# Kernel optimization log

Measured on AMD Instinct MI355X. Metric: run time of the kernel, lower is better.

Reference implementation:

```python
import jax, jax.numpy as jnp
import numpy as np
import math

B, T, C, TF, N, DK = 4, 2048, 768, 128, 8, 96  # DK = max(C//8,16)

def _tau_init(Tw):
    alpha = 0.1 ** (1.0 / max(Tw - 1, 1))
    tau = -math.log(max(alpha, 1e-10))
    return math.log(math.exp(tau) - 1 + 1e-10)

def setup_inputs() -> dict:
    key = jax.random.key(0)
    ks = jax.random.split(key, 13)
    w = lambda k, shp: jax.random.normal(k, shp, jnp.float32) * 0.02
    return {
        'x': jax.random.normal(ks[0], (B, T, C), jnp.float32),
        'tau_gate': jnp.float32(_tau_init(max(T // 2, 4))),
        'tau_fast': jnp.float32(_tau_init(TF)),
        'tau_slow': jnp.float32(_tau_init(T)),
        'Wp': w(ks[1], (C, C)), 'bp': jnp.zeros((C,), jnp.float32),
        'Wxf': w(ks[2], (C, C)), 'bxf': jnp.full((C,), -0.5, jnp.float32),
        'Wxs': w(ks[3], (C, C)), 'bxs': jnp.full((C,), 0.5, jnp.float32),
        'Wcf': w(ks[4], (C, C)), 'Wcs': w(ks[5], (C, C)),
        'Wq': w(ks[6], (DK, C)), 'Wk': w(ks[7], (DK, C)),
        'Wfast': w(ks[8], (C, C)), 'bfast': jnp.zeros((C,), jnp.float32),
        'Wslow': w(ks[9], (C, C)), 'bslow': jnp.zeros((C,), jnp.float32),
        'Wsoma': w(ks[10], (C, C)), 'bsoma': jnp.zeros((C,), jnp.float32),
        'Wanc': w(ks[11], (C, C)), 'banc': jnp.zeros((C,), jnp.float32),
        'anchor_scales': jnp.linspace(1.5, -1.5, N).astype(jnp.float32),
        'blend_raw': jnp.zeros((1,), jnp.float32),
        'ln_g': jnp.ones((C,), jnp.float32), 'ln_b': jnp.zeros((C,), jnp.float32),
    }

def _lin(x, W, b=None):
    # torch Linear: y = x @ W.T + b, W is (out, in)
    y = jnp.einsum('btc,oc->bto', x, W)
    return y if b is None else y + b

def _ema(b, tau_raw):
    # exact h_t = alpha*h_{t-1} + b_t, h_{-1}=0 (same math as full causal conv with kernel alpha^j)
    alpha = jnp.exp(-jax.nn.softplus(tau_raw))
    def step(h, bt):
        h = alpha * h + bt
        return h, h
    _, hs = jax.lax.scan(step, jnp.zeros_like(b[:, 0, :]), jnp.swapaxes(b, 0, 1))
    return jnp.swapaxes(hs, 0, 1)  # (B,T,C)

def _forward(x, tau_gate, tau_fast, tau_slow, Wp, bp, Wxf, bxf, Wxs, bxs, Wcf, Wcs,
             Wq, Wk, Wfast, bfast, Wslow, bslow, Wsoma, bsoma, Wanc, banc,
             anchor_scales, blend_raw, ln_g, ln_b):
    x_proj = jnp.tanh(_lin(x, Wp, bp))
    ctx_gate = _ema(x, tau_gate)
    wg_f = jax.nn.sigmoid(_lin(x, Wxf, bxf) + _lin(ctx_gate, Wcf))
    wg_s = jax.nn.sigmoid(_lin(x, Wxs, bxs) + _lin(ctx_gate, Wcs))
    ctx_fast = _ema(x_proj * wg_f, tau_fast)
    ctx_slow = _ema(x_proj * wg_s, tau_slow)
    # F1 content gate: causal max-score sigmoid
    q = _lin(x, Wq)
    k = _lin(x, Wk)
    sc = jnp.einsum('btd,bsd->bts', q, k) * (DK ** -0.5)
    tril = jnp.tril(jnp.ones((T, T), bool))
    sc = jnp.where(tril[None], sc, -jnp.inf)
    cg = jax.nn.sigmoid(jnp.max(sc, axis=-1, keepdims=True))  # (B,T,1)
    ctx_fast = ctx_fast * cg
    ctx_slow = ctx_slow * cg
    # F5 anchors (static positions)
    pos = np.array([min(i * (T // N), T - 1) for i in range(N)])
    a = jnp.tanh(jnp.einsum('bnc,oc->bno', x[:, pos, :], Wanc) + banc)  # (B,N,C)
    delta = jnp.einsum('n,bnc->bc', jax.nn.sigmoid(anchor_scales), a)
    ctx_fast = ctx_fast + delta[:, None, :]
    ctx_slow = ctx_slow + delta[:, None, :]
    # F6 blend of fast/slow gates (torch.lerp)
    bl = jax.nn.sigmoid(blend_raw)  # (1,)
    gf = jax.nn.sigmoid(_lin(ctx_fast, Wfast, bfast))
    gs = jax.nn.sigmoid(_lin(ctx_slow, Wslow, bslow))
    gate = gf + bl * (gs - gf)
    soma = jnp.tanh(_lin(x, Wsoma, bsoma))
    y = soma * gate
    mu = jnp.mean(y, -1, keepdims=True)
    var = jnp.var(y, -1, keepdims=True)
    return (y - mu) / jnp.sqrt(var + 1e-5) * ln_g + ln_b  # dropout p=0 -> identity

def reference(x, tau_gate, tau_fast, tau_slow, Wp, bp, Wxf, bxf, Wxs, bxs, Wcf, Wcs,
              Wq, Wk, Wfast, bfast, Wslow, bslow, Wsoma, bsoma, Wanc, banc,
              anchor_scales, blend_raw, ln_g, ln_b):
    return _forward(x, tau_gate, tau_fast, tau_slow, Wp, bp, Wxf, bxf, Wxs, bxs, Wcf, Wcs,
                    Wq, Wk, Wfast, bfast, Wslow, bslow, Wsoma, bsoma, Wanc, banc,
                    anchor_scales, blend_raw, ln_g, ln_b)
```

## Files before the change

### kernel.cpp

```cpp
#include <hip/hip_runtime.h>
#include <math.h>

#define B_ 4
#define T_ 2048
#define C_ 768
#define DK_ 96
#define NA_ 8
#define M_ (B_*T_)
#define K2_ (2*C_)
#define NCH_ 256
#define CK_ 8

typedef __attribute__((ext_vector_type(8))) _Float16 half8;
typedef __attribute__((ext_vector_type(4))) _Float16 half4;
typedef __attribute__((ext_vector_type(4))) float floatx4;

#define AS1 __attribute__((address_space(1)))
#define AS3 __attribute__((address_space(3)))

__device__ __forceinline__ float sigm(float x){ return 1.f/(1.f + expf(-x)); }
__device__ __forceinline__ unsigned enc_max(float f){
  unsigned i = __float_as_uint(f);
  return (i & 0x80000000u) ? ~i : (i | 0x80000000u);
}
__device__ __forceinline__ float dec_max(unsigned u){
  unsigned i = (u & 0x80000000u) ? (u & 0x7FFFFFFFu) : ~u;
  return __uint_as_float(i);
}
__device__ __forceinline__ void gld16(const _Float16* g, _Float16* l){
  __builtin_amdgcn_global_load_lds((const AS1 unsigned int*)g, (AS3 unsigned int*)l, 16, 0, 0);
}

__global__ __launch_bounds__(192) void k_castx(
    const float* __restrict__ x, const float* __restrict__ tau,
    _Float16* __restrict__ xh, float* __restrict__ Sg){
  float al = expf(-log1pf(expf(tau[0])));
  int blk = blockIdx.x, b = blk >> 8, ch = blk & (NCH_-1);
  int t0 = b*T_ + ch*CK_;
  int c4 = threadIdx.x;
  float s0=0.f,s1=0.f,s2=0.f,s3=0.f;
  #pragma unroll
  for (int t = 0; t < CK_; ++t){
    float4 v = *(const float4*)(x + (size_t)(t0+t)*C_ + c4*4);
    half4 h = { (_Float16)v.x,(_Float16)v.y,(_Float16)v.z,(_Float16)v.w };
    *(half4*)(xh + (size_t)(t0+t)*C_ + c4*4) = h;
    s0 = al*s0 + v.x; s1 = al*s1 + v.y; s2 = al*s2 + v.z; s3 = al*s3 + v.w;
  }
  float4 sv = { s0,s1,s2,s3 };
  *(float4*)(Sg + (size_t)blk*C_ + c4*4) = sv;
}

#define NB0 4608
#define NB1 4896
#define NB2 4920
#define NB3 4932
__global__ __launch_bounds__(256) void k_prep(
    const float* __restrict__ x,
    const float* __restrict__ Wp, const float* __restrict__ Wfast,
    const float* __restrict__ Wslow, const float* __restrict__ Wsoma,
    const float* __restrict__ Wxf, const float* __restrict__ Wxs,
    const float* __restrict__ Wcf, const float* __restrict__ Wcs,
    const float* __restrict__ Wq, const float* __restrict__ Wk,
    const float* __restrict__ Wanc, const float* __restrict__ banc,
    const float* __restrict__ ascl, const float* __restrict__ tau_gate,
    const float* __restrict__ Sg,
    _Float16* __restrict__ wall, _Float16* __restrict__ wqk,
    unsigned* __restrict__ cgE, float* __restrict__ Hg, float* __restrict__ dlt)
{
  __shared__ float xs[NA_*C_];
  __shared__ float part[NA_*128];
  int blk = blockIdx.x, tid = threadIdx.x;
  if (blk < NB0){
    int i = blk*256 + tid;
    const int per = (C_*C_)/4;
    int s = i / per, j = i - s*per;
    const float* src = s==0?Wp : s==1?Wfast : s==2?Wslow : s==3?Wsoma
                     : s==4?Wxf : s==5?Wxs : s==6?Wcf : Wcs;
    float4 v = ((const float4*)src)[j];
    half4 h = { (_Float16)v.x, (_Float16)v.y, (_Float16)v.z, (_Float16)v.w };
    ((half4*)wall)[(size_t)s*per + j] = h;
  } else if (blk < NB1){
    int sub = blk - NB0;
    if (sub >= 256){ cgE[(sub-256)*256 + tid] = 0u; return; }
    const float* src = (sub < 96) ? Wq + (size_t)sub*C_
                     : (sub < 192 ? Wk + (size_t)(sub-96)*C_ : nullptr);
    #pragma unroll
    for (int k = 0; k < 3; ++k){
      int c = tid + k*256;
      wqk[(size_t)sub*C_ + c] = src ? (_Float16)src[c] : (_Float16)0.f;
    }
  } else if (blk < NB2){
    int ab = blk - NB1;
    int ct = ab % 6, b = ab / 6;
    for (int i = tid; i < NA_*C_; i += 256){
      int n = i / C_, c = i - n*C_;
      xs[i] = x[(size_t)(b*T_ + n*(T_/NA_))*C_ + c];
    }
    __syncthreads();
    int col = ct*128 + (tid & 127), kh = tid >> 7;
    float acc[NA_] = {0,0,0,0,0,0,0,0};
    const float* wrow = Wanc + (size_t)col*C_ + kh*384;
    const float* xk = xs + kh*384;
    for (int k = 0; k < 384; ++k){
      float wv = wrow[k];
      #pragma unroll
      for (int n = 0; n < NA_; ++n) acc[n] += xk[n*C_ + k]*wv;
    }
    if (kh){
      #pragma unroll
      for (int n = 0; n < NA_; ++n) part[n*128 + (tid & 127)] = acc[n];
    }
    __syncthreads();
    if (!kh){
      float d = 0.f;
      float bv = banc[col];
      #pragma unroll
      for (int n = 0; n < NA_; ++n){
        float a = tanhf(acc[n] + part[n*128 + (tid & 127)] + bv);
        d += sigm(ascl[n]) * a;
      }
      dlt[(size_t)b*C_ + col] = d;
    }
  } else {
    int sub = blk - NB2;
    int b = sub / 3, c = (sub - b*3)*256 + tid;
    float aCK = expf(-(float)CK_ * log1pf(expf(tau_gate[0])));
    float h = 0.f;
    for (int ch = 0; ch < NCH_; ++ch){
      size_t idx = (size_t)(b*NCH_ + ch)*C_ + c;
      Hg[idx] = h;
      h = aCK*h + Sg[idx];
    }
  }
}

__global__ __launch_bounds__(256) void k_p2_fs(const float* __restrict__ Sf, const float* __restrict__ Ss,
                                               float* __restrict__ Hf, float* __restrict__ Hs,
                                               const float* __restrict__ tf, const float* __restrict__ ts){
  int blk = blockIdx.x;
  int which = blk / 12, sub = blk - which*12;
  int b = sub / 3, c = (sub - b*3)*256 + threadIdx.x;
  const float* S = which ? Ss : Sf;
  float* H = which ? Hs : Hf;
  float aCK = expf(-(float)CK_ * log1pf(expf(which ? ts[0] : tf[0])));
  float h = 0.f;
  for (int ch = 0; ch < NCH_; ++ch){
    size_t idx = (size_t)(b*NCH_ + ch)*C_ + c;
    H[idx] = h;
    h = aCK*h + S[idx];
  }
}

__global__ __launch_bounds__(192) void k_gate_p3(
    const _Float16* __restrict__ xh, const float* __restrict__ H,
    const float* __restrict__ tau, _Float16* __restrict__ gate){
  float al = expf(-log1pf(expf(tau[0])));
  int blk = blockIdx.x, b = blk >> 8, ch = blk & (NCH_-1);
  int c4 = threadIdx.x;
  float4 h0 = *(const float4*)(H + (size_t)blk*C_ + c4*4);
  float g0=h0.x, g1=h0.y, g2=h0.z, g3=h0.w;
  int t0 = b*T_ + ch*CK_;
  #pragma unroll
  for (int t = 0; t < CK_; ++t){
    half4 v = *(const half4*)(xh + (size_t)(t0+t)*C_ + c4*4);
    g0 = al*g0 + (float)v[0]; g1 = al*g1 + (float)v[1];
    g2 = al*g2 + (float)v[2]; g3 = al*g3 + (float)v[3];
    half4 o = { (_Float16)g0,(_Float16)g1,(_Float16)g2,(_Float16)g3 };
    *(half4*)(gate + (size_t)(t0+t)*C_ + c4*4) = o;
  }
}

__device__ __forceinline__ void stage_tile(const _Float16* __restrict__ src, int stride,
                                           int r0, int k0, _Float16* lds){
  int tid = threadIdx.x;
  int wave = tid >> 6, lane = tid & 63;
  #pragma unroll
  for (int it = 0; it < 4; ++it){
    int cb = it*256 + wave*64;
    int ck = cb + lane;
    int row = ck >> 3;
    int kp = (ck & 7) ^ (row & 7);
    gld16(src + (size_t)(r0+row)*stride + k0 + kp*8, lds + (size_t)cb*8);
  }
}

__device__ __forceinline__ void mfma_pass(const _Float16* As, const _Float16* Ws, floatx4 acc[4][4]){
  int tid = threadIdx.x;
  int wave = tid >> 6, lane = tid & 63;
  int wr = wave >> 1, wc = wave & 1;
  int lr = lane & 15, lq = lane >> 4;
  #pragma unroll
  for (int ks = 0; ks < 2; ++ks){
    half8 fa[4], fb[4];
    int off = (((ks*4 + lq) ^ (lr & 7)) << 3);
    #pragma unroll
    for (int i = 0; i < 4; ++i){
      fa[i] = *(const half8*)(As + (wr*64 + i*16 + lr)*64 + off);
      fb[i] = *(const half8*)(Ws + (wc*64 + i*16 + lr)*64 + off);
    }
    #pragma unroll
    for (int i = 0; i < 4; ++i)
      #pragma unroll
      for (int j = 0; j < 4; ++j)
        acc[i][j] = __builtin_amdgcn_mfma_f32_16x16x32_f16(fa[i], fb[j], acc[i][j], 0, 0, 0);
  }
}

__device__ __forceinline__ void store_tile_f16(floatx4 acc[4][4], _Float16* __restrict__ out, int ldo,
                                               const float* bias, const float* bias2,
                                               int m0, int n0, int act){
  int tid = threadIdx.x;
  int wave = tid >> 6, lane = tid & 63;
  int wr = wave >> 1, wc = wave & 1;
  int lr = lane & 15, lq = lane >> 4;
  #pragma unroll
  for (int i = 0; i < 4; ++i){
    #pragma unroll
    for (int j = 0; j < 4; ++j){
      int col = n0 + wc*64 + j*16 + lr;
      float bv = 0.f;
      if (bias) bv = (bias2 && col >= C_) ? bias2[col - C_] : bias[col];
      #pragma unroll
      for (int r = 0; r < 4; ++r){
        int rowm = m0 + wr*64 + i*16 + lq*4 + r;
        float z = acc[i][j][r] + bv;
        if (act == 1) z = tanhf(z);
        else if (act == 2) z = sigm(z);
        out[(size_t)rowm*ldo + col] = (_Float16)z;
      }
    }
  }
}

__global__ __launch_bounds__(256,4) void k_gemm_s3(
    const _Float16* __restrict__ xh, const _Float16* __restrict__ gate,
    const _Float16* __restrict__ wall, const _Float16* __restrict__ wqk,
    const float* __restrict__ bp, const float* __restrict__ bxf, const float* __restrict__ bxs,
    _Float16* __restrict__ xph, _Float16* __restrict__ wgfs, _Float16* __restrict__ qk)
{
  __shared__ _Float16 As[128*64];
  __shared__ _Float16 Ws[128*64];
  const size_t per = (size_t)C_*C_;
  floatx4 acc[4][4] = {};
  int m0 = blockIdx.x * 128;
  int ny = blockIdx.y;
  if (ny < 6){
    for (int k0 = 0; k0 < C_; k0 += 64){
      stage_tile(xh, C_, m0, k0, As);
      stage_tile(wall, C_, ny*128, k0, Ws);
      asm volatile("s_waitcnt vmcnt(0)" ::: "memory");
      __syncthreads();
      mfma_pass(As, Ws, acc);
      __syncthreads();
    }
    store_tile_f16(acc, xph, C_, bp, nullptr, m0, ny*128, 1);
  } else if (ny < 18){
    int n0 = (ny-6)*128;
    for (int k0 = 0; k0 < C_; k0 += 64){
      stage_tile(xh, C_, m0, k0, As);
      stage_tile(wall + 4*per, C_, n0, k0, Ws);
      asm volatile("s_waitcnt vmcnt(0)" ::: "memory");
      __syncthreads();
      mfma_pass(As, Ws, acc);
      __syncthreads();
    }
    for (int k0 = 0; k0 < C_; k0 += 64){
      stage_tile(gate, C_, m0, k0, As);
      stage_tile(wall + 6*per, C_, n0, k0, Ws);
      asm volatile("s_waitcnt vmcnt(0)" ::: "memory");
      __syncthreads();
      mfma_pass(As, Ws, acc);
      __syncthreads();
    }
    store_tile_f16(acc, wgfs, K2_, bxf, bxs, m0, n0, 2);
  } else {
    int n0 = (ny-18)*128;
    for (int k0 = 0; k0 < C_; k0 += 64){
      stage_tile(xh, C_, m0, k0, As);
      stage_tile(wqk, C_, n0, k0, Ws);
      asm volatile("s_waitcnt vmcnt(0)" ::: "memory");
      __syncthreads();
      mfma_pass(As, Ws, acc);
      __syncthreads();
    }
    store_tile_f16(acc, qk, 256, nullptr, nullptr, m0, n0, 0);
  }
}

__global__ __launch_bounds__(256,3) void k_gemm_s7(
    const _Float16* __restrict__ xph, const _Float16* __restrict__ wgfs,
    const _Float16* __restrict__ xh, const _Float16* __restrict__ wall,
    const float* __restrict__ Hf, const float* __restrict__ Hs,
    const float* __restrict__ tau_fast, const float* __restrict__ tau_slow,
    const unsigned* __restrict__ cgE, const float* __restrict__ dlt,
    const float* __restrict__ bf, const float* __restrict__ bs, const float* __restrict__ bso,
    _Float16* __restrict__ gfb, _Float16* __restrict__ gsb, _Float16* __restrict__ somab)
{
  __shared__ _Float16 As[128*64];
  __shared__ _Float16 Wg[128*64];
  __shared__ _Float16 Bs[128*64];
  __shared__ float cgv[128];
  const size_t per = (size_t)C_*C_;
  floatx4 acc[4][4] = {};
  int m0 = blockIdx.x * 128;
  int s = blockIdx.y / 6, nt = (blockIdx.y % 6) * 128;
  int tid = threadIdx.x;
  if (s == 2){
    for (int k0 = 0; k0 < C_; k0 += 64){
      stage_tile(xh, C_, m0, k0, As);
      stage_tile(wall + 3*per, C_, nt, k0, Bs);
      asm volatile("s_waitcnt vmcnt(0)" ::: "memory");
      __syncthreads();
      mfma_pass(As, Bs, acc);
      __syncthreads();
    }
    store_tile_f16(acc, somab, C_, bso, nullptr, m0, nt, 1);
  } else {
    float al = expf(-log1pf(expf(s ? tau_slow[0] : tau_fast[0])));
    const float* Hx = s ? Hs : Hf;
    const _Float16* wsrc = wgfs + (s ? C_ : 0);
    const _Float16* Wm = wall + (size_t)(s+1)*per;
    int b = m0 >> 11;
    int ch0 = (m0 & (T_-1)) >> 3;
    if (tid < 128) cgv[tid] = sigm(dec_max(cgE[m0 + tid]));
    __syncthreads();
    int rc = tid >> 4, cc = (tid >> 1) & 7, hh = tid & 1;
    for (int k0 = 0; k0 < C_; k0 += 64){
      stage_tile(xph, C_, m0, k0, As);
      stage_tile(wsrc, K2_, m0, k0, Wg);
      stage_tile(Wm, C_, nt, k0, Bs);
      asm volatile("s_waitcnt vmcnt(0)" ::: "memory");
      __syncthreads();
      {
        float4 hv = *(const float4*)(Hx + ((size_t)b*NCH_ + ch0 + rc)*C_ + k0 + cc*8 + hh*4);
        float4 d  = *(const float4*)(dlt + (size_t)b*C_ + k0 + cc*8 + hh*4);
        float e0=hv.x, e1=hv.y, e2=hv.z, e3=hv.w;
        #pragma unroll
        for (int r = 0; r < 8; ++r){
          int idx = (rc*8+r)*64 + ((cc^r)<<3) + hh*4;
          half4 p = *(const half4*)(As+idx);
          half4 wv = *(const half4*)(Wg+idx);
          e0 = al*e0 + (float)p[0]*(float)wv[0];
          e1 = al*e1 + (float)p[1]*(float)wv[1];
          e2 = al*e2 + (float)p[2]*(float)wv[2];
          e3 = al*e3 + (float)p[3]*(float)wv[3];
          float cgr = cgv[rc*8 + r];
          half4 o = { (_Float16)(e0*cgr + d.x), (_Float16)(e1*cgr + d.y),
                      (_Float16)(e2*cgr + d.z), (_Float16)(e3*cgr + d.w) };
          *(half4*)(As+idx) = o;
        }
      }
      __syncthreads();
      mfma_pass(As, Bs, acc);
      __syncthreads();
    }
    store_tile_f16(acc, s ? gsb : gfb, C_, s ? bs : bf, nullptr, m0, nt, 2);
  }
}

#define SLDK 104
__global__ __launch_bounds__(256,3) void k_score_fs(
    const _Float16* __restrict__ qk, unsigned* __restrict__ cgE,
    const _Float16* __restrict__ xp, const _Float16* __restrict__ wgfs,
    const float* __restrict__ tf, const float* __restrict__ ts,
    float* __restrict__ Sf, float* __restrict__ Ss)
{
  __shared__ _Float16 Qs[128*SLDK];
  __shared__ _Float16 Ks[128*SLDK];
  __shared__ float sred[256];
  int idx = blockIdx.x;
  int tid = threadIdx.x;
  if (idx >= 544){
    if (tid >= 192) return;
    int f = idx - 544;
    float af = expf(-log1pf(expf(tf[0])));
    float as = expf(-log1pf(expf(ts[0])));
    int b = f >> 8, ch = f & (NCH_-1);
    int t0 = b*T_ + ch*CK_;
    float f0=0,f1=0,f2=0,f3=0, s0=0,s1=0,s2=0,s3=0;
    #pragma unroll
    for (int t = 0; t < CK_; ++t){
      half4 p = *(const half4*)(xp + (size_t)(t0+t)*C_ + tid*4);
      half4 wf = *(const half4*)(wgfs + (size_t)(t0+t)*K2_ + tid*4);
      half4 ws = *(const half4*)(wgfs + (size_t)(t0+t)*K2_ + C_ + tid*4);
      f0 = af*f0 + (float)p[0]*(float)wf[0]; s0 = as*s0 + (float)p[0]*(float)ws[0];
      f1 = af*f1 + (float)p[1]*(float)wf[1]; s1 = as*s1 + (float)p[1]*(float)ws[1];
      f2 = af*f2 + (float)p[2]*(float)wf[2]; s2 = as*s2 + (float)p[2]*(float)ws[2];
      f3 = af*f3 + (float)p[3]*(float)wf[3]; s3 = as*s3 + (float)p[3]*(float)ws[3];
    }
    float4 fv = { f0,f1,f2,f3 }, sv = { s0,s1,s2,s3 };
    *(float4*)(Sf + (size_t)f*C_ + tid*4) = fv;
    *(float4*)(Ss + (size_t)f*C_ + tid*4) = sv;
    return;
  }
  int b = idx / 136;
  int p = idx - b*136;
  int ti = (int)((sqrtf(8.f*p + 1.f) - 1.f)*0.5f);
  while ((ti+1)*(ti+2)/2 <= p) ++ti;
  while (ti*(ti+1)/2 > p) --ti;
  int sj = p - ti*(ti+1)/2;

  const _Float16* qg = qk + (size_t)(b*T_ + ti*128)*256;
  const _Float16* kg = qk + (size_t)(b*T_ + sj*128)*256 + 96;
  #pragma unroll
  for (int r = 0; r < 6; ++r){
    int ci = tid + r*256;
    int row = ci / 12, kp = ci % 12;
    *(uint4*)(&Qs[row*SLDK + kp*8]) = *(const uint4*)(qg + (size_t)row*256 + kp*8);
    *(uint4*)(&Ks[row*SLDK + kp*8]) = *(const uint4*)(kg + (size_t)row*256 + kp*8);
  }
  __syncthreads();

  int wave = tid >> 6, lane = tid & 63;
  int wr = wave >> 1, wc = wave & 1;
  int lr = lane & 15, lq = lane >> 4;
  floatx4 acc[4][4] = {};
  #pragma unroll
  for (int ks = 0; ks < 3; ++ks){
    half8 fa[4], fb[4];
    #pragma unroll
    for (int i = 0; i < 4; ++i){
      fa[i] = *(const half8*)(&Qs[(wr*64 + i*16 + lr)*SLDK + ks*32 + lq*8]);
      fb[i] = *(const half8*)(&Ks[(wc*64 + i*16 + lr)*SLDK + ks*32 + lq*8]);
    }
    #pragma unroll
    for (int i = 0; i < 4; ++i)
      #pragma unroll
      for (int j = 0; j < 4; ++j)
        acc[i][j] = __builtin_amdgcn_mfma_f32_16x16x32_f16(fa[i], fb[j], acc[i][j], 0, 0, 0);
  }
  const float scale = 0.10206207f;
  #pragma unroll
  for (int i = 0; i < 4; ++i){
    #pragma unroll
    for (int r = 0; r < 4; ++r){
      int row64 = i*16 + lq*4 + r;
      int tg = ti*128 + wr*64 + row64;
      float v = -3.0e38f;
      #pragma unroll
      for (int j = 0; j < 4; ++j){
        int sg = sj*128 + wc*64 + j*16 + lr;
        if (sg <= tg) v = fmaxf(v, acc[i][j][r]*scale);
      }
      #pragma unroll
      for (int off = 1; off < 16; off <<= 1) v = fmaxf(v, __shfl_xor(v, off, 16));
      if (lr == 0) sred[wr*128 + wc*64 + row64] = v;
    }
  }
  __syncthreads();
  if (wc == 0 && lane < 64){
    int row64 = lane;
    float v = fmaxf(sred[wr*128 + row64], sred[wr*128 + 64 + row64]);
    int tg = ti*128 + wr*64 + row64;
    atomicMax(&cgE[(size_t)b*T_ + tg], enc_max(v));
  }
}

__global__ __launch_bounds__(256) void k_ln(const _Float16* __restrict__ gfb,
                                            const _Float16* __restrict__ gsb,
                                            const _Float16* __restrict__ somab,
                                            const float* __restrict__ blendr,
                                            const float* __restrict__ g, const float* __restrict__ be,
                                            float* __restrict__ out){
  int wave = threadIdx.x >> 6, lane = threadIdx.x & 63;
  int row = blockIdx.x*4 + wave;
  float bl = sigm(blendr[0]);
  size_t rb = (size_t)row*C_;
  float v[12];
  float s = 0.f, ss = 0.f;
  #pragma unroll
  for (int w2 = 0; w2 < 3; ++w2){
    size_t o = rb + w2*256 + lane*4;
    half4 gf4 = *(const half4*)(gfb + o);
    half4 gs4 = *(const half4*)(gsb + o);
    half4 so4 = *(const half4*)(somab + o);
    #pragma unroll
    for (int i = 0; i < 4; ++i){
      float gf = (float)gf4[i], gs = (float)gs4[i], so = (float)so4[i];
      float y = so * (gf + bl*(gs - gf));
      v[w2*4 + i] = y; s += y; ss += y*y;
    }
  }
  #pragma unroll
  for (int off = 1; off < 64; off <<= 1){ s += __shfl_xor(s, off); ss += __shfl_xor(ss, off); }
  float mu  = s * (1.f/C_);
  float var = ss * (1.f/C_) - mu*mu;
  float inv = rsqrtf(var + 1e-5f);
  #pragma unroll
  for (int w2 = 0; w2 < 3; ++w2){
    int c0 = w2*256 + lane*4;
    float4 o4;
    o4.x = (v[w2*4+0]-mu)*inv*g[c0+0] + be[c0+0];
    o4.y = (v[w2*4+1]-mu)*inv*g[c0+1] + be[c0+1];
    o4.z = (v[w2*4+2]-mu)*inv*g[c0+2] + be[c0+2];
    o4.w = (v[w2*4+3]-mu)*inv*g[c0+3] + be[c0+3];
    *(float4*)(out + rb + c0) = o4;
  }
}

extern "C" void kernel_launch(void* const* d_in, const int* in_sizes, int n_in,
                              void* d_out, int out_size, void* d_ws, size_t ws_size,
                              hipStream_t stream){
  (void)in_sizes; (void)n_in; (void)out_size;
  const float* x        = (const float*)d_in[0];
  const float* tau_gate = (const float*)d_in[1];
  const float* tau_fast = (const float*)d_in[2];
  const float* tau_slow = (const float*)d_in[3];
  const float* Wp   = (const float*)d_in[4];  const float* bp    = (const float*)d_in[5];
  const float* Wxf  = (const float*)d_in[6];  const float* bxf   = (const float*)d_in[7];
  const float* Wxs  = (const float*)d_in[8];  const float* bxs   = (const float*)d_in[9];
  const float* Wcf  = (const float*)d_in[10]; const float* Wcs   = (const float*)d_in[11];
  const float* Wq   = (const float*)d_in[12]; const float* Wk    = (const float*)d_in[13];
  const float* Wfast= (const float*)d_in[14]; const float* bfast = (const float*)d_in[15];
  const float* Wslow= (const float*)d_in[16]; const float* bslow = (const float*)d_in[17];
  const float* Wsoma= (const float*)d_in[18]; const float* bsoma = (const float*)d_in[19];
  const float* Wanc = (const float*)d_in[20]; const float* banc  = (const float*)d_in[21];
  const float* ascl = (const float*)d_in[22]; const float* blendr= (const float*)d_in[23];
  const float* lng  = (const float*)d_in[24]; const float* lnb   = (const float*)d_in[25];
  float* out = (float*)d_out;

  char* w = (char*)d_ws;
  auto alloc = [&](size_t bytes)->void*{
    void* p = (void*)w; w += (bytes + 255) & ~(size_t)255; return p;
  };
  _Float16* xh    = (_Float16*)alloc((size_t)M_*C_*2);
  _Float16* wall  = (_Float16*)alloc((size_t)8*C_*C_*2);
  _Float16* wqk   = (_Float16*)alloc((size_t)256*C_*2);
  _Float16* xph   = (_Float16*)alloc((size_t)M_*C_*2);
  _Float16* wgfs  = (_Float16*)alloc((size_t)M_*K2_*2);
  _Float16* qk    = (_Float16*)alloc((size_t)M_*256*2);
  _Float16* gfb   = (_Float16*)alloc((size_t)M_*C_*2);
  _Float16* gsb   = (_Float16*)alloc((size_t)M_*C_*2);
  _Float16* somab = (_Float16*)alloc((size_t)M_*C_*2);
  unsigned* cgE   = (unsigned*)alloc((size_t)M_*4);
  float* Sg = (float*)alloc((size_t)B_*NCH_*C_*4);
  float* Hg = (float*)alloc((size_t)B_*NCH_*C_*4);
  float* Ss = (float*)alloc((size_t)B_*NCH_*C_*4);
  float* Hs = (float*)alloc((size_t)B_*NCH_*C_*4);
  float* dlt = (float*)alloc((size_t)B_*C_*4);
  _Float16* gate = gfb;
  float* Sf = Sg;
  float* Hf = Hg;
  if ((size_t)(w - (char*)d_ws) > ws_size) return;

  k_castx<<<B_*NCH_, 192, 0, stream>>>(x, tau_gate, xh, Sg);
  k_prep<<<NB3, 256, 0, stream>>>(x, Wp, Wfast, Wslow, Wsoma, Wxf, Wxs, Wcf, Wcs, Wq, Wk,
                                  Wanc, banc, ascl, tau_gate, Sg, wall, wqk, cgE, Hg, dlt);
  k_gate_p3<<<B_*NCH_, 192, 0, stream>>>(xh, Hg, tau_gate, gate);
  k_gemm_s3<<<dim3(M_/128, 20), 256, 0, stream>>>(xh, gate, wall, wqk,
                                                  bp, bxf, bxs, xph, wgfs, qk);
  k_score_fs<<<544 + B_*NCH_, 256, 0, stream>>>(qk, cgE, xph, wgfs, tau_fast, tau_slow, Sf, Ss);
  k_p2_fs<<<2*B_*3, 256, 0, stream>>>(Sf, Ss, Hf, Hs, tau_fast, tau_slow);
  k_gemm_s7<<<dim3(M_/128, 18), 256, 0, stream>>>(xph, wgfs, xh, wall, Hf, Hs,
                                                  tau_fast, tau_slow, cgE, dlt,
                                                  bfast, bslow, bsoma, gfb, gsb, somab);
  k_ln<<<M_/4, 256, 0, stream>>>(gfb, gsb, somab, blendr, lng, lnb, out);
}
```

Before: 354.0 us.

## Parallelize chunk-carry scans and move fast/slow EMA out of final GEMM

The serial chunk-carry scans over 256 chunks are replaced by a two-level scan. Each block handles 16 channels, with 16 thread groups each scanning 16 chunks and combining carries through shared memory, so far more blocks run in parallel. The per-K-tile fast/slow EMA prologue in k_gemm_s7 moves into a separate elementwise kernel that writes the gated contexts in place into wgfs. The GEMM becomes a plain A×B loop with smaller LDS use and higher occupancy. The cost is an extra kernel launch and an extra global read/write pass over the fast/slow activations.

```diff
diff --git a/kernel.cpp b/kernel.cpp
--- a/kernel.cpp
+++ b/kernel.cpp
@@ -31,6 +31,30 @@
   __builtin_amdgcn_global_load_lds((const AS1 unsigned int*)g, (AS3 unsigned int*)l, 16, 0, 0);
 }
 
+__device__ __forceinline__ void scan2l(const float* __restrict__ S, float* __restrict__ H,
+                                       int b, int cg0, float aCK, float A16,
+                                       float* __restrict__ carry ){
+  int tid = threadIdx.x;
+  int cl = tid & 15, g = tid >> 4;
+  int c = cg0 + cl;
+  float sv[16];
+  float cv = 0.f;
+  #pragma unroll
+  for (int j = 0; j < 16; ++j){
+    sv[j] = S[(size_t)(b*NCH_ + g*16 + j)*C_ + c];
+    cv = aCK*cv + sv[j];
+  }
+  carry[cl*17 + g] = cv;
+  __syncthreads();
+  float h = 0.f;
+  for (int gp = 0; gp < g; ++gp) h = A16*h + carry[cl*17 + gp];
+  #pragma unroll
+  for (int j = 0; j < 16; ++j){
+    H[(size_t)(b*NCH_ + g*16 + j)*C_ + c] = h;
+    h = aCK*h + sv[j];
+  }
+}
+
 __global__ __launch_bounds__(192) void k_castx(
     const float* __restrict__ x, const float* __restrict__ tau,
     _Float16* __restrict__ xh, float* __restrict__ Sg){
@@ -53,7 +77,7 @@
 #define NB0 4608
 #define NB1 4896
 #define NB2 4920
-#define NB3 4932
+#define NB3 5112
 __global__ __launch_bounds__(256) void k_prep(
     const float* __restrict__ x,
     const float* __restrict__ Wp, const float* __restrict__ Wfast,
@@ -69,6 +93,7 @@
 {
   __shared__ float xs[NA_*C_];
   __shared__ float part[NA_*128];
+  __shared__ float carry[16*17];
   int blk = blockIdx.x, tid = threadIdx.x;
   if (blk < NB0){
     int i = blk*256 + tid;
@@ -123,32 +148,22 @@
     }
   } else {
     int sub = blk - NB2;
-    int b = sub / 3, c = (sub - b*3)*256 + tid;
-    float aCK = expf(-(float)CK_ * log1pf(expf(tau_gate[0])));
-    float h = 0.f;
-    for (int ch = 0; ch < NCH_; ++ch){
-      size_t idx = (size_t)(b*NCH_ + ch)*C_ + c;
-      Hg[idx] = h;
-      h = aCK*h + Sg[idx];
-    }
+    int b = sub / 48, cg0 = (sub - b*48)*16;
+    float sp = log1pf(expf(tau_gate[0]));
+    scan2l(Sg, Hg, b, cg0, expf(-8.f*sp), expf(-128.f*sp), carry);
   }
 }
 
 __global__ __launch_bounds__(256) void k_p2_fs(const float* __restrict__ Sf, const float* __restrict__ Ss,
                                                float* __restrict__ Hf, float* __restrict__ Hs,
                                                const float* __restrict__ tf, const float* __restrict__ ts){
+  __shared__ float carry[16*17];
   int blk = blockIdx.x;
-  int which = blk / 12, sub = blk - which*12;
-  int b = sub / 3, c = (sub - b*3)*256 + threadIdx.x;
-  const float* S = which ? Ss : Sf;
-  float* H = which ? Hs : Hf;
-  float aCK = expf(-(float)CK_ * log1pf(expf(which ? ts[0] : tf[0])));
-  float h = 0.f;
-  for (int ch = 0; ch < NCH_; ++ch){
-    size_t idx = (size_t)(b*NCH_ + ch)*C_ + c;
-    H[idx] = h;
-    h = aCK*h + S[idx];
-  }
+  int which = blk / (B_*48);
+  int rem = blk - which*(B_*48);
+  int b = rem / 48, cg0 = (rem - b*48)*16;
+  float sp = log1pf(expf(which ? ts[0] : tf[0]));
+  scan2l(which ? Ss : Sf, which ? Hs : Hf, b, cg0, expf(-8.f*sp), expf(-128.f*sp), carry);
 }
 
 __global__ __launch_bounds__(192) void k_gate_p3(
@@ -167,6 +182,44 @@
     g2 = al*g2 + (float)v[2]; g3 = al*g3 + (float)v[3];
     half4 o = { (_Float16)g0,(_Float16)g1,(_Float16)g2,(_Float16)g3 };
     *(half4*)(gate + (size_t)(t0+t)*C_ + c4*4) = o;
+  }
+}
+
+__global__ __launch_bounds__(192) void k_fs_p3(
+    const _Float16* __restrict__ xph, _Float16* __restrict__ wgfs,
+    const float* __restrict__ Hf, const float* __restrict__ Hs,
+    const float* __restrict__ tf, const float* __restrict__ ts,
+    const unsigned* __restrict__ cgE, const float* __restrict__ dlt){
+  float af = expf(-log1pf(expf(tf[0])));
+  float as = expf(-log1pf(expf(ts[0])));
+  int blk = blockIdx.x, b = blk >> 8, ch = blk & (NCH_-1);
+  int c4 = threadIdx.x;
+  int t0 = b*T_ + ch*CK_;
+  float4 hf4 = *(const float4*)(Hf + (size_t)blk*C_ + c4*4);
+  float4 hs4 = *(const float4*)(Hs + (size_t)blk*C_ + c4*4);
+  float4 d4  = *(const float4*)(dlt + (size_t)b*C_ + c4*4);
+  float f0=hf4.x, f1=hf4.y, f2=hf4.z, f3=hf4.w;
+  float e0=hs4.x, e1=hs4.y, e2=hs4.z, e3=hs4.w;
+  float cgr[CK_];
+  #pragma unroll
+  for (int t = 0; t < CK_; ++t) cgr[t] = sigm(dec_max(cgE[t0+t]));
+  #pragma unroll
+  for (int t = 0; t < CK_; ++t){
+    size_t rp = (size_t)(t0+t);
+    half4 p  = *(const half4*)(xph  + rp*C_  + c4*4);
+    half4 wf = *(const half4*)(wgfs + rp*K2_ + c4*4);
+    half4 ws = *(const half4*)(wgfs + rp*K2_ + C_ + c4*4);
+    f0 = af*f0 + (float)p[0]*(float)wf[0]; e0 = as*e0 + (float)p[0]*(float)ws[0];
+    f1 = af*f1 + (float)p[1]*(float)wf[1]; e1 = as*e1 + (float)p[1]*(float)ws[1];
+    f2 = af*f2 + (float)p[2]*(float)wf[2]; e2 = as*e2 + (float)p[2]*(float)ws[2];
+    f3 = af*f3 + (float)p[3]*(float)wf[3]; e3 = as*e3 + (float)p[3]*(float)ws[3];
+    float cg = cgr[t];
+    half4 of = { (_Float16)(f0*cg + d4.x), (_Float16)(f1*cg + d4.y),
+                 (_Float16)(f2*cg + d4.z), (_Float16)(f3*cg + d4.w) };
+    half4 os = { (_Float16)(e0*cg + d4.x), (_Float16)(e1*cg + d4.y),
+                 (_Float16)(e2*cg + d4.z), (_Float16)(e3*cg + d4.w) };
+    *(half4*)(wgfs + rp*K2_ + c4*4) = of;
+    *(half4*)(wgfs + rp*K2_ + C_ + c4*4) = os;
   }
 }
 
@@ -287,75 +340,32 @@
   }
 }
 
-__global__ __launch_bounds__(256,3) void k_gemm_s7(
-    const _Float16* __restrict__ xph, const _Float16* __restrict__ wgfs,
-    const _Float16* __restrict__ xh, const _Float16* __restrict__ wall,
-    const float* __restrict__ Hf, const float* __restrict__ Hs,
-    const float* __restrict__ tau_fast, const float* __restrict__ tau_slow,
-    const unsigned* __restrict__ cgE, const float* __restrict__ dlt,
+__global__ __launch_bounds__(256,4) void k_gemm_s7(
+    const _Float16* __restrict__ cfs, const _Float16* __restrict__ xh,
+    const _Float16* __restrict__ wall,
     const float* __restrict__ bf, const float* __restrict__ bs, const float* __restrict__ bso,
     _Float16* __restrict__ gfb, _Float16* __restrict__ gsb, _Float16* __restrict__ somab)
 {
   __shared__ _Float16 As[128*64];
-  __shared__ _Float16 Wg[128*64];
   __shared__ _Float16 Bs[128*64];
-  __shared__ float cgv[128];
   const size_t per = (size_t)C_*C_;
   floatx4 acc[4][4] = {};
   int m0 = blockIdx.x * 128;
   int s = blockIdx.y / 6, nt = (blockIdx.y % 6) * 128;
-  int tid = threadIdx.x;
-  if (s == 2){
-    for (int k0 = 0; k0 < C_; k0 += 64){
-      stage_tile(xh, C_, m0, k0, As);
-      stage_tile(wall + 3*per, C_, nt, k0, Bs);
-      asm volatile("s_waitcnt vmcnt(0)" ::: "memory");
-      __syncthreads();
-      mfma_pass(As, Bs, acc);
-      __syncthreads();
-    }
-    store_tile_f16(acc, somab, C_, bso, nullptr, m0, nt, 1);
-  } else {
-    float al = expf(-log1pf(expf(s ? tau_slow[0] : tau_fast[0])));
-    const float* Hx = s ? Hs : Hf;
-    const _Float16* wsrc = wgfs + (s ? C_ : 0);
-    const _Float16* Wm = wall + (size_t)(s+1)*per;
-    int b = m0 >> 11;
-    int ch0 = (m0 & (T_-1)) >> 3;
-    if (tid < 128) cgv[tid] = sigm(dec_max(cgE[m0 + tid]));
+  const _Float16* Asrc = (s == 0) ? cfs : (s == 1 ? cfs + C_ : xh);
+  int lda = (s == 2) ? C_ : K2_;
+  const _Float16* Bsrc = wall + (size_t)(s+1)*per;
+  for (int k0 = 0; k0 < C_; k0 += 64){
+    stage_tile(Asrc, lda, m0, k0, As);
+    stage_tile(Bsrc, C_, nt, k0, Bs);
+    asm volatile("s_waitcnt vmcnt(0)" ::: "memory");
     __syncthreads();
-    int rc = tid >> 4, cc = (tid >> 1) & 7, hh = tid & 1;
-    for (int k0 = 0; k0 < C_; k0 += 64){
-      stage_tile(xph, C_, m0, k0, As);
-      stage_tile(wsrc, K2_, m0, k0, Wg);
-      stage_tile(Wm, C_, nt, k0, Bs);
-      asm volatile("s_waitcnt vmcnt(0)" ::: "memory");
-      __syncthreads();
-      {
-        float4 hv = *(const float4*)(Hx + ((size_t)b*NCH_ + ch0 + rc)*C_ + k0 + cc*8 + hh*4);
-        float4 d  = *(const float4*)(dlt + (size_t)b*C_ + k0 + cc*8 + hh*4);
-        float e0=hv.x, e1=hv.y, e2=hv.z, e3=hv.w;
-        #pragma unroll
-        for (int r = 0; r < 8; ++r){
-          int idx = (rc*8+r)*64 + ((cc^r)<<3) + hh*4;
-          half4 p = *(const half4*)(As+idx);
-          half4 wv = *(const half4*)(Wg+idx);
-          e0 = al*e0 + (float)p[0]*(float)wv[0];
-          e1 = al*e1 + (float)p[1]*(float)wv[1];
-          e2 = al*e2 + (float)p[2]*(float)wv[2];
-          e3 = al*e3 + (float)p[3]*(float)wv[3];
-          float cgr = cgv[rc*8 + r];
-          half4 o = { (_Float16)(e0*cgr + d.x), (_Float16)(e1*cgr + d.y),
-                      (_Float16)(e2*cgr + d.z), (_Float16)(e3*cgr + d.w) };
-          *(half4*)(As+idx) = o;
-        }
-      }
-      __syncthreads();
-      mfma_pass(As, Bs, acc);
-      __syncthreads();
-    }
-    store_tile_f16(acc, s ? gsb : gfb, C_, s ? bs : bf, nullptr, m0, nt, 2);
-  }
+    mfma_pass(As, Bs, acc);
+    __syncthreads();
+  }
+  if (s == 2)      store_tile_f16(acc, somab, C_, bso, nullptr, m0, nt, 1);
+  else if (s == 1) store_tile_f16(acc, gsb,  C_, bs,  nullptr, m0, nt, 2);
+  else             store_tile_f16(acc, gfb,  C_, bf,  nullptr, m0, nt, 2);
 }
 
 #define SLDK 104
@@ -550,9 +560,9 @@
   k_gemm_s3<<<dim3(M_/128, 20), 256, 0, stream>>>(xh, gate, wall, wqk,
                                                   bp, bxf, bxs, xph, wgfs, qk);
   k_score_fs<<<544 + B_*NCH_, 256, 0, stream>>>(qk, cgE, xph, wgfs, tau_fast, tau_slow, Sf, Ss);
-  k_p2_fs<<<2*B_*3, 256, 0, stream>>>(Sf, Ss, Hf, Hs, tau_fast, tau_slow);
-  k_gemm_s7<<<dim3(M_/128, 18), 256, 0, stream>>>(xph, wgfs, xh, wall, Hf, Hs,
-                                                  tau_fast, tau_slow, cgE, dlt,
+  k_p2_fs<<<2*B_*48, 256, 0, stream>>>(Sf, Ss, Hf, Hs, tau_fast, tau_slow);
+  k_fs_p3<<<B_*NCH_, 192, 0, stream>>>(xph, wgfs, Hf, Hs, tau_fast, tau_slow, cgE, dlt);
+  k_gemm_s7<<<dim3(M_/128, 18), 256, 0, stream>>>(wgfs, xh, wall,
                                                   bfast, bslow, bsoma, gfb, gsb, somab);
   k_ln<<<M_/4, 256, 0, stream>>>(gfb, gsb, somab, blendr, lng, lnb, out);
 }
```

New measurement: 419.9 us. +18.6%, slower.
